# Optimization experiments

Hardware: AMD Instinct MI355X
Metric: run time of the kernel (lower is better)

## Reference

```python
import jax, jax.numpy as jnp
import numpy as np
from jax import lax

K = 9  # 3x3 kernel points


def _gather(feat, iy, ix):
    """feat: [B,C,H,W]; iy,ix: [B,K,H,W] int32. Zero padding outside bounds.
    Returns [B,C,K,H,W]."""
    B, C, H, W = feat.shape
    valid = ((iy >= 0) & (iy < H) & (ix >= 0) & (ix < W))
    iyc = jnp.clip(iy, 0, H - 1)
    ixc = jnp.clip(ix, 0, W - 1)
    flat = (iyc * W + ixc).reshape(B, 1, -1)            # [B,1,K*H*W]
    g = jnp.take_along_axis(feat.reshape(B, C, H * W), flat, axis=2)
    g = g.reshape(B, C, K, H, W)
    return g * valid[:, None].astype(feat.dtype)


def _bilinear(feat, ys, xs):
    """feat: [B,C,H,W]; ys,xs: [B,K,H,W] float sampling coords -> [B,C,K,H,W]."""
    y0 = jnp.floor(ys)
    x0 = jnp.floor(xs)
    wy = (ys - y0)[:, None]
    wx = (xs - x0)[:, None]
    y0i = y0.astype(jnp.int32)
    x0i = x0.astype(jnp.int32)
    y1i = y0i + 1
    x1i = x0i + 1
    v00 = _gather(feat, y0i, x0i)
    v01 = _gather(feat, y0i, x1i)
    v10 = _gather(feat, y1i, x0i)
    v11 = _gather(feat, y1i, x1i)
    return (v00 * (1 - wy) * (1 - wx) + v01 * (1 - wy) * wx
            + v10 * wy * (1 - wx) + v11 * wy * wx)


def _deform_layer(x, w_off, b_off, w, b, dilation=1):
    """Modulated deformable 3x3 conv, stride 1, padding=dilation (same size)."""
    B, C, H, W = x.shape
    # offset/mask conv (regular 3x3 conv, same padding)
    om = lax.conv_general_dilated(
        x, w_off, window_strides=(1, 1),
        padding=[(dilation, dilation), (dilation, dilation)],
        rhs_dilation=(dilation, dilation),
        dimension_numbers=('NCHW', 'OIHW', 'NCHW')) + b_off[None, :, None, None]
    off = om[:, :2 * K].reshape(B, K, 2, H, W)   # (dy, dx) per kernel point
    mask = jax.nn.sigmoid(om[:, 2 * K:])         # [B,K,H,W]
    dy = off[:, :, 0]
    dx = off[:, :, 1]
    # base kernel grid offsets (-d, 0, +d)
    ky, kx = jnp.meshgrid(jnp.arange(3), jnp.arange(3), indexing='ij')
    base_y = ((ky.reshape(-1) - 1) * dilation).astype(x.dtype)   # [K]
    base_x = ((kx.reshape(-1) - 1) * dilation).astype(x.dtype)
    gy = jnp.arange(H, dtype=x.dtype)
    gx = jnp.arange(W, dtype=x.dtype)
    ys = gy[None, None, :, None] + base_y[None, :, None, None] + dy  # [B,K,H,W]
    xs = gx[None, None, None, :] + base_x[None, :, None, None] + dx
    sampled = _bilinear(x, ys, xs) * mask[:, None]   # [B,C,K,H,W]
    wk = w.reshape(w.shape[0], w.shape[1], K)        # [O,I,K]
    out = jnp.einsum('bikhw,oik->bohw', sampled, wk) + b[None, :, None, None]
    return out


def setup_inputs() -> dict:
    key = jax.random.key(0)
    ks = jax.random.split(key, 16)
    B, C, H, W = 4, 256, 64, 64
    O = 256
    inp = {'x': jax.random.normal(ks[0], (B, C, H, W), jnp.float32)}
    chans = [(C, C), (C, O), (O, O)]  # layer i==num_layers-2 maps in->out
    for i, (ci, co) in enumerate(chans):
        k = jax.random.split(ks[i + 1], 4)
        # offset conv: 27 = 3*K channels (18 offsets + 9 masks); small init
        inp[f'w_off{i}'] = jax.random.normal(k[0], (3 * K, ci, 3, 3), jnp.float32) * 0.01
        inp[f'b_off{i}'] = jnp.zeros((3 * K,), jnp.float32)
        # deform conv weight: kaiming normal, fan_in = ci*K
        std = np.sqrt(2.0 / (ci * K)).astype(np.float32)
        inp[f'w{i}'] = jax.random.normal(k[1], (co, ci, 3, 3), jnp.float32) * std
        inp[f'b{i}'] = jnp.zeros((co,), jnp.float32)
    return inp


def reference(x, w_off0, b_off0, w0, b0, w_off1, b_off1, w1, b1,
              w_off2, b_off2, w2, b2):
    params = [(w_off0, b_off0, w0, b0),
              (w_off1, b_off1, w1, b1),
              (w_off2, b_off2, w2, b2)]
    for (wo, bo, w, b) in params:
        x = jax.nn.relu(_deform_layer(x, wo, bo, w, b, dilation=1))
    return x
```

## Files before the change

kernel.cpp:

```cpp
#include <hip/hip_runtime.h>
#include <math.h>

#define Bn 4
#define Cn 256
#define Hn 64
#define Wn 64
#define On 256
#define HWn 4096
#define Pn 16384
#define Kc 2304

#define LGKM0 0xc07f

typedef _Float16 half8 __attribute__((ext_vector_type(8)));
typedef float floatx4 __attribute__((ext_vector_type(4)));

__global__ void k_init(const float* __restrict__ x, _Float16* __restrict__ act0,
                       const float* __restrict__ w0, const float* __restrict__ w1,
                       const float* __restrict__ w2, const float* __restrict__ wo0,
                       const float* __restrict__ wo1, const float* __restrict__ wo2,
                       _Float16* __restrict__ wtp, _Float16* __restrict__ wbop) {
  int bx = blockIdx.x;
  int tid = threadIdx.x;
  if (bx < 4096) {
    __shared__ float tile[32][33];
    int cx = bx & 127, cy = (bx >> 7) & 7, b = bx >> 10;
    int c0 = cx * 32, r0 = cy * 32;
    int tx = tid & 31, ty = tid >> 5;
    const float* ib = x + (size_t)b * Cn * HWn;
    _Float16* ob = act0 + (size_t)b * Cn * HWn;
#pragma unroll
    for (int i = 0; i < 32; i += 8)
      tile[ty + i][tx] = ib[(size_t)(r0 + ty + i) * HWn + (c0 + tx)];
    __syncthreads();
#pragma unroll
    for (int i = 0; i < 32; i += 8)
      ob[(size_t)(c0 + ty + i) * Cn + (r0 + tx)] = (_Float16)tile[tx][ty + i];
  } else if (bx < 4864) {
    int b2 = bx - 4096;
    int l = b2 >> 8;
    int n = b2 & 255;
    const float* w = (l == 0) ? w0 : (l == 1) ? w1 : w2;
    _Float16* dst = wtp + (size_t)l * 256 * Kc;
    int g = n >> 4, col = n & 15;
    int cq = tid >> 6;
    int kk = tid & 63;
    int kq = kk >> 5;
    int k32 = kk & 31;
    int quad = k32 >> 3;
    int e = k32 & 7;
    const float* src = w + (size_t)n * 2304 + (size_t)tid * 9;
#pragma unroll
    for (int t = 0; t < 9; ++t) {
      int c = t * 4 + cq;
      size_t d = ((size_t)((c * 16 + g) * 2 + kq)) * 512 + (quad * 16 + col) * 8 + e;
      dst[d] = (_Float16)src[t];
    }
  } else {
    int b3 = bx - 4864;
    int l = b3 >> 5;
    int n = b3 & 31;
    const float* w = (l == 0) ? wo0 : (l == 1) ? wo1 : wo2;
    _Float16* dst = wbop + (size_t)l * 36 * 2048;
    int g = n >> 4, col = n & 15;
    int cw = tid >> 6;
    int r = tid & 63;
    int kq = r >> 5;
    int r2 = r & 31;
    int quad = r2 >> 3;
    int e = r2 & 7;
#pragma unroll
    for (int t = 0; t < 9; ++t) {
      int c = t * 4 + cw;
      size_t d = ((size_t)((c * 2 + g) * 2 + kq)) * 512 + (quad * 16 + col) * 8 + e;
      dst[d] = (n < 27) ? (_Float16)w[((size_t)n * 256 + tid) * 9 + t] : (_Float16)0.f;
    }
  }
}

__global__ __launch_bounds__(512) void k_layer(
    const _Float16* __restrict__ xh,
    const _Float16* __restrict__ wbop, const float* __restrict__ boff,
    const _Float16* __restrict__ wtp, const float* __restrict__ bias,
    _Float16* __restrict__ outh, float* __restrict__ outf) {
  __shared__ __align__(16) _Float16 As[2][64][72];
  __shared__ __align__(16) _Float16 Bs[2][16384];
  __shared__ __align__(16) float omS[64 * 33];
  __shared__ __align__(16) float sampS[64][9][8];

  int bid = blockIdx.x;
  int lb = ((bid & 7) << 5) + (bid >> 3);
  int p0 = lb * 64;
  int tid = threadIdx.x;
  int lane = tid & 63;
  int wave = tid >> 6;
  int quad = lane >> 4;
  int col = lane & 15;

  int ar = tid >> 3;
  int aci = (tid & 7) * 8;

  int p = p0 + ar;
  int bimg = p >> 12;
  int yx = p & 4095;
  int y = yx >> 6, x = yx & 63;

  half8 zero8;
#pragma unroll
  for (int e = 0; e < 8; ++e) zero8[e] = (_Float16)0.f;

  int mi = wave >> 1;
  int ng = wave & 1;

  floatx4 acc1 = (floatx4){0.f, 0.f, 0.f, 0.f};
  half8 ga;
  half8 bos0, bos1;
  int abase = 0;
  bool avalid = false;
  {
    int sy = y - 1, sx = x - 1;
    avalid = (sy >= 0) & (sy < Hn) & (sx >= 0) & (sx < Wn);
    abase = (((bimg * Hn + (avalid ? sy : 0)) * Wn) + (avalid ? sx : 0)) * Cn;
    ga = zero8;
    if (avalid) ga = *(const half8*)(xh + (size_t)abase + aci);
    bos0 = zero8; bos1 = zero8;
    if (tid < 256) {
      bos0 = *(const half8*)(wbop + (size_t)tid * 8);
      bos1 = *(const half8*)(wbop + 2048 + (size_t)tid * 8);
    }
  }

#pragma unroll 1
  for (int t = 0; t < 9; ++t) {
#pragma unroll
    for (int cc = 0; cc < 4; ++cc) {
      *(half8*)&As[cc & 1][ar][aci] = ga;
      if (tid < 256)
        *(half8*)&Bs[cc & 1][tid * 8] = (cc & 1) ? bos1 : bos0;
      if (cc < 3) {
        ga = zero8;
        if (avalid) ga = *(const half8*)(xh + (size_t)abase + (cc + 1) * 64 + aci);
      } else if (t < 8) {
        int tn = t + 1;
        int sy = y + tn / 3 - 1;
        int sx = x + tn % 3 - 1;
        avalid = (sy >= 0) & (sy < Hn) & (sx >= 0) & (sx < Wn);
        abase = (((bimg * Hn + (avalid ? sy : 0)) * Wn) + (avalid ? sx : 0)) * Cn;
        ga = zero8;
        if (avalid) ga = *(const half8*)(xh + (size_t)abase + aci);
      }
      if ((cc < 2 || t < 8) && tid < 256) {
        half8 v = *(const half8*)(wbop + ((size_t)(4 * t) + cc + 2) * 2048 + tid * 8);
        if (cc & 1) bos1 = v; else bos0 = v;
      }

      __builtin_amdgcn_s_waitcnt(LGKM0);
      __builtin_amdgcn_s_barrier();

#pragma unroll
      for (int kq = 0; kq < 2; ++kq) {
        half8 af = *(const half8*)&As[cc & 1][mi * 16 + col][kq * 32 + quad * 8];
        half8 bf = *(const half8*)&Bs[cc & 1][(ng * 2 + kq) * 512 + lane * 8];
        acc1 = __builtin_amdgcn_mfma_f32_16x16x32_f16(af, bf, acc1, 0, 0, 0);
      }
    }
  }

  {
    int n1 = ng * 16 + col;
    if (n1 < 27) {
      float bb = boff[n1];
#pragma unroll
      for (int r = 0; r < 4; ++r)
        omS[(mi * 16 + quad * 4 + r) * 33 + n1] = acc1[r] + bb;
    }
  }
  __syncthreads();

  for (int e = tid; e < 576; e += 512) {
    int lp = e / 9;
    int k = e - lp * 9;
    int pp = p0 + lp;
    int bi = pp >> 12;
    int pyx = pp & 4095;
    int py = pyx >> 6, px = pyx & 63;

    float dy = omS[lp * 33 + 2 * k];
    float dx = omS[lp * 33 + 2 * k + 1];
    float m = 1.f / (1.f + expf(-omS[lp * 33 + 18 + k]));

    float ys = (float)(py + k / 3 - 1) + dy;
    float xs = (float)(px + k % 3 - 1) + dx;
    float y0f = floorf(ys), x0f = floorf(xs);
    float wy = ys - y0f, wx = xs - x0f;
    int y0 = (int)y0f, x0 = (int)x0f;
    int y1 = y0 + 1, x1 = x0 + 1;

    bool vy0 = (y0 >= 0) & (y0 < Hn);
    bool vy1 = (y1 >= 0) & (y1 < Hn);
    bool vx0 = (x0 >= 0) & (x0 < Wn);
    bool vx1 = (x1 >= 0) & (x1 < Wn);
    int y0c = min(max(y0, 0), Hn - 1), y1c = min(max(y1, 0), Hn - 1);
    int x0c = min(max(x0, 0), Wn - 1), x1c = min(max(x1, 0), Wn - 1);

    int base = bi * HWn;
    float* s = &sampS[lp][k][0];
    ((int*)s)[0] = (base + y0c * Wn + x0c) * Cn;
    ((int*)s)[1] = (base + y0c * Wn + x1c) * Cn;
    ((int*)s)[2] = (base + y1c * Wn + x0c) * Cn;
    ((int*)s)[3] = (base + y1c * Wn + x1c) * Cn;
    s[4] = (vy0 && vx0) ? m * (1.f - wy) * (1.f - wx) : 0.f;
    s[5] = (vy0 && vx1) ? m * (1.f - wy) * wx : 0.f;
    s[6] = (vy1 && vx0) ? m * wy * (1.f - wx) : 0.f;
    s[7] = (vy1 && vx1) ? m * wy * wx : 0.f;
  }
  __syncthreads();

  int mw = wave >> 2;
  int nw = wave & 3;

  float bj[4];
#pragma unroll
  for (int j = 0; j < 4; ++j) bj[j] = bias[(nw * 4 + j) * 16 + col];

  floatx4 acc[2][4];
#pragma unroll
  for (int i = 0; i < 2; ++i)
#pragma unroll
    for (int j = 0; j < 4; ++j) acc[i][j] = (floatx4){0.f, 0.f, 0.f, 0.f};

  half8 g00, g01, g10, g11;
  half8 bst0[4], bst1[4];
  int4 ofsC, ofsN;
  float4 wvC, wvN;

  ofsC = *(const int4*)&sampS[ar][0][0];
  wvC = *(const float4*)&sampS[ar][0][4];
  ofsN = ofsC; wvN = wvC;
  g00 = *(const half8*)(xh + (size_t)ofsC.x + aci);
  g01 = *(const half8*)(xh + (size_t)ofsC.y + aci);
  g10 = *(const half8*)(xh + (size_t)ofsC.z + aci);
  g11 = *(const half8*)(xh + (size_t)ofsC.w + aci);
#pragma unroll
  for (int q = 0; q < 4; ++q)
    bst0[q] = *(const half8*)(wtp + (size_t)(q * 512 + tid) * 8);
#pragma unroll
  for (int q = 0; q < 4; ++q)
    bst1[q] = *(const half8*)(wtp + 16384 + (size_t)(q * 512 + tid) * 8);

#pragma unroll 1
  for (int t = 0; t < 9; ++t) {
    if (t < 8) {
      ofsN = *(const int4*)&sampS[ar][t + 1][0];
      wvN = *(const float4*)&sampS[ar][t + 1][4];
    }
#pragma unroll
    for (int cc = 0; cc < 4; ++cc) {
      {
        _Float16 h00 = (_Float16)wvC.x, h01 = (_Float16)wvC.y;
        _Float16 h10 = (_Float16)wvC.z, h11 = (_Float16)wvC.w;
        half8 r;
#pragma unroll
        for (int e = 0; e < 8; ++e)
          r[e] = g00[e] * h00 + g01[e] * h01 + g10[e] * h10 + g11[e] * h11;
        *(half8*)&As[cc & 1][ar][aci] = r;
      }
#pragma unroll
      for (int q = 0; q < 4; ++q)
        *(half8*)&Bs[cc & 1][(q * 512 + tid) * 8] = (cc & 1) ? bst1[q] : bst0[q];
      if (cc < 3) {
        int ci = (cc + 1) * 64 + aci;
        g00 = *(const half8*)(xh + (size_t)ofsC.x + ci);
        g01 = *(const half8*)(xh + (size_t)ofsC.y + ci);
        g10 = *(const half8*)(xh + (size_t)ofsC.z + ci);
        g11 = *(const half8*)(xh + (size_t)ofsC.w + ci);
      } else if (t < 8) {
        g00 = *(const half8*)(xh + (size_t)ofsN.x + aci);
        g01 = *(const half8*)(xh + (size_t)ofsN.y + aci);
        g10 = *(const half8*)(xh + (size_t)ofsN.z + aci);
        g11 = *(const half8*)(xh + (size_t)ofsN.w + aci);
      }
      if (cc < 2 || t < 8) {
        const _Float16* wsrc = wtp + ((size_t)(4 * t) + cc + 2) * 16384;
#pragma unroll
        for (int q = 0; q < 4; ++q) {
          half8 v = *(const half8*)(wsrc + (size_t)(q * 512 + tid) * 8);
          if (cc & 1) bst1[q] = v; else bst0[q] = v;
        }
      }

      __builtin_amdgcn_s_waitcnt(LGKM0);
      __builtin_amdgcn_s_barrier();

      half8 af[2][2];
#pragma unroll
      for (int kq = 0; kq < 2; ++kq)
#pragma unroll
        for (int i = 0; i < 2; ++i)
          af[kq][i] =
              *(const half8*)&As[cc & 1][mw * 32 + i * 16 + col][kq * 32 + quad * 8];

      half8 bf[2][4];
#pragma unroll
      for (int kq = 0; kq < 2; ++kq)
#pragma unroll
        for (int j = 0; j < 4; ++j)
          bf[kq][j] =
              *(const half8*)&Bs[cc & 1][((nw * 4 + j) * 2 + kq) * 512 + lane * 8];

#pragma unroll
      for (int kq = 0; kq < 2; ++kq)
#pragma unroll
        for (int i = 0; i < 2; ++i)
#pragma unroll
          for (int j = 0; j < 4; ++j)
            acc[i][j] = __builtin_amdgcn_mfma_f32_16x16x32_f16(
                af[kq][i], bf[kq][j], acc[i][j], 0, 0, 0);
    }
    ofsC = ofsN;
    wvC = wvN;
  }

#pragma unroll
  for (int i = 0; i < 2; ++i)
#pragma unroll
    for (int j = 0; j < 4; ++j) {
      int n = (nw * 4 + j) * 16 + col;
      if (outf) {
        int pb = p0 + mw * 32 + i * 16 + quad * 4;
        int bi = pb >> 12;
        int pyx = pb & 4095;
        float4 v;
        v.x = fmaxf(acc[i][j][0] + bj[j], 0.f);
        v.y = fmaxf(acc[i][j][1] + bj[j], 0.f);
        v.z = fmaxf(acc[i][j][2] + bj[j], 0.f);
        v.w = fmaxf(acc[i][j][3] + bj[j], 0.f);
        *(float4*)(outf + ((size_t)(bi * On + n)) * HWn + pyx) = v;
      } else {
#pragma unroll
        for (int r = 0; r < 4; ++r) {
          int pp = p0 + mw * 32 + i * 16 + quad * 4 + r;
          float v = fmaxf(acc[i][j][r] + bj[j], 0.f);
          outh[(size_t)pp * On + n] = (_Float16)v;
        }
      }
    }
}

extern "C" void kernel_launch(void* const* d_in, const int* in_sizes, int n_in,
                              void* d_out, int out_size, void* d_ws, size_t ws_size,
                              hipStream_t stream) {
  (void)in_sizes; (void)n_in; (void)out_size; (void)ws_size;
  const float* x = (const float*)d_in[0];

  _Float16* act0h = (_Float16*)d_ws;
  _Float16* act1h = act0h + (size_t)Pn * Cn;
  _Float16* wbop  = act1h + (size_t)Pn * Cn;
  _Float16* wtp   = wbop + (size_t)3 * 36 * 2048;

  k_init<<<4960, 256, 0, stream>>>(
      x, act0h,
      (const float*)d_in[3], (const float*)d_in[7], (const float*)d_in[11],
      (const float*)d_in[1], (const float*)d_in[5], (const float*)d_in[9],
      wtp, wbop);

  _Float16* cur = act0h;
  _Float16* nxt = act1h;
  for (int l = 0; l < 3; ++l) {
    const float* b_off = (const float*)d_in[2 + l * 4];
    const float* b     = (const float*)d_in[4 + l * 4];
    k_layer<<<Pn / 64, 512, 0, stream>>>(
        cur, wbop + (size_t)l * 36 * 2048, b_off,
        wtp + (size_t)l * 256 * Kc, b, nxt,
        (l == 2) ? (float*)d_out : nullptr);
    _Float16* tswap = cur; cur = nxt; nxt = tswap;
  }
}
```

Before: 232.3 us.

## Split k_layer into producer waves for gather and weight staging at 1024 threads

Doubles the block to 1024 threads and specializes them. The first 512 threads do the bilinear gather or offset-conv A loads, and the other 512 load weight tiles into shared memory. The main MFMA tile is redistributed over 16 waves, each computing 2x2 fragments instead of 2x4. The aim is to overlap global weight loads with gathers and add more waves to hide latency, at the cost of more barrier participants, fewer accumulators per wave and tighter register limits from launch_bounds(1024,4).

```diff
diff --git a/kernel.cpp b/kernel.cpp
--- a/kernel.cpp
+++ b/kernel.cpp
@@ -78,7 +78,7 @@
   }
 }
 
-__global__ __launch_bounds__(512) void k_layer(
+__global__ __launch_bounds__(1024, 4) void k_layer(
     const _Float16* __restrict__ xh,
     const _Float16* __restrict__ wbop, const float* __restrict__ boff,
     const _Float16* __restrict__ wtp, const float* __restrict__ bias,
@@ -97,8 +97,10 @@
   int quad = lane >> 4;
   int col = lane & 15;
 
-  int ar = tid >> 3;
+  bool isA = tid < 512;
+  int ar = (tid & 511) >> 3;
   int aci = (tid & 7) * 8;
+  int t2 = tid & 511;
 
   int p = p0 + ar;
   int bimg = p >> 12;
@@ -109,64 +111,71 @@
 #pragma unroll
   for (int e = 0; e < 8; ++e) zero8[e] = (_Float16)0.f;
 
-  int mi = wave >> 1;
+  int mi = (wave & 7) >> 1;
   int ng = wave & 1;
 
   floatx4 acc1 = (floatx4){0.f, 0.f, 0.f, 0.f};
-  half8 ga;
-  half8 bos0, bos1;
+  half8 ga = zero8;
+  half8 bos0 = zero8, bos1 = zero8;
   int abase = 0;
   bool avalid = false;
+  bool isBo = (tid >= 512) && (tid < 768);
   {
     int sy = y - 1, sx = x - 1;
     avalid = (sy >= 0) & (sy < Hn) & (sx >= 0) & (sx < Wn);
     abase = (((bimg * Hn + (avalid ? sy : 0)) * Wn) + (avalid ? sx : 0)) * Cn;
-    ga = zero8;
-    if (avalid) ga = *(const half8*)(xh + (size_t)abase + aci);
-    bos0 = zero8; bos1 = zero8;
-    if (tid < 256) {
-      bos0 = *(const half8*)(wbop + (size_t)tid * 8);
-      bos1 = *(const half8*)(wbop + 2048 + (size_t)tid * 8);
-    }
-  }
+    if (isA && avalid) ga = *(const half8*)(xh + (size_t)abase + aci);
+    if (isBo) {
+      bos0 = *(const half8*)(wbop + (size_t)t2 * 8);
+      bos1 = *(const half8*)(wbop + 2048 + (size_t)t2 * 8);
+    }
+  }
+
+  _Float16* Bo0 = &Bs[0][0];
+  _Float16* Bo1 = &Bs[0][2048];
 
 #pragma unroll 1
   for (int t = 0; t < 9; ++t) {
 #pragma unroll
     for (int cc = 0; cc < 4; ++cc) {
-      *(half8*)&As[cc & 1][ar][aci] = ga;
-      if (tid < 256)
-        *(half8*)&Bs[cc & 1][tid * 8] = (cc & 1) ? bos1 : bos0;
-      if (cc < 3) {
-        ga = zero8;
-        if (avalid) ga = *(const half8*)(xh + (size_t)abase + (cc + 1) * 64 + aci);
-      } else if (t < 8) {
-        int tn = t + 1;
-        int sy = y + tn / 3 - 1;
-        int sx = x + tn % 3 - 1;
-        avalid = (sy >= 0) & (sy < Hn) & (sx >= 0) & (sx < Wn);
-        abase = (((bimg * Hn + (avalid ? sy : 0)) * Wn) + (avalid ? sx : 0)) * Cn;
-        ga = zero8;
-        if (avalid) ga = *(const half8*)(xh + (size_t)abase + aci);
-      }
-      if ((cc < 2 || t < 8) && tid < 256) {
-        half8 v = *(const half8*)(wbop + ((size_t)(4 * t) + cc + 2) * 2048 + tid * 8);
+      if (isA) {
+        *(half8*)&As[cc & 1][ar][aci] = ga;
+      } else if (isBo) {
+        *(half8*)&((cc & 1) ? Bo1 : Bo0)[t2 * 8] = (cc & 1) ? bos1 : bos0;
+      }
+      if (isA) {
+        if (cc < 3) {
+          ga = zero8;
+          if (avalid) ga = *(const half8*)(xh + (size_t)abase + (cc + 1) * 64 + aci);
+        } else if (t < 8) {
+          int tn = t + 1;
+          int sy = y + tn / 3 - 1;
+          int sx = x + tn % 3 - 1;
+          avalid = (sy >= 0) & (sy < Hn) & (sx >= 0) & (sx < Wn);
+          abase = (((bimg * Hn + (avalid ? sy : 0)) * Wn) + (avalid ? sx : 0)) * Cn;
+          ga = zero8;
+          if (avalid) ga = *(const half8*)(xh + (size_t)abase + aci);
+        }
+      } else if (isBo && (cc < 2 || t < 8)) {
+        half8 v = *(const half8*)(wbop + ((size_t)(4 * t) + cc + 2) * 2048 + t2 * 8);
         if (cc & 1) bos1 = v; else bos0 = v;
       }
 
       __builtin_amdgcn_s_waitcnt(LGKM0);
       __builtin_amdgcn_s_barrier();
 
-#pragma unroll
-      for (int kq = 0; kq < 2; ++kq) {
-        half8 af = *(const half8*)&As[cc & 1][mi * 16 + col][kq * 32 + quad * 8];
-        half8 bf = *(const half8*)&Bs[cc & 1][(ng * 2 + kq) * 512 + lane * 8];
-        acc1 = __builtin_amdgcn_mfma_f32_16x16x32_f16(af, bf, acc1, 0, 0, 0);
-      }
-    }
-  }
-
-  {
+      if (isA) {
+#pragma unroll
+        for (int kq = 0; kq < 2; ++kq) {
+          half8 af = *(const half8*)&As[cc & 1][mi * 16 + col][kq * 32 + quad * 8];
+          half8 bf = *(const half8*)&((cc & 1) ? Bo1 : Bo0)[(ng * 2 + kq) * 512 + lane * 8];
+          acc1 = __builtin_amdgcn_mfma_f32_16x16x32_f16(af, bf, acc1, 0, 0, 0);
+        }
+      }
+    }
+  }
+
+  if (isA) {
     int n1 = ng * 16 + col;
     if (n1 < 27) {
       float bb = boff[n1];
@@ -177,7 +186,8 @@
   }
   __syncthreads();
 
-  for (int e = tid; e < 576; e += 512) {
+  if (tid < 576) {
+    int e = tid;
     int lp = e / 9;
     int k = e - lp * 9;
     int pp = p0 + lp;
@@ -216,47 +226,50 @@
   }
   __syncthreads();
 
-  int mw = wave >> 2;
-  int nw = wave & 3;
-
-  float bj[4];
-#pragma unroll
-  for (int j = 0; j < 4; ++j) bj[j] = bias[(nw * 4 + j) * 16 + col];
-
-  floatx4 acc[2][4];
+  int mw = wave >> 3;
+  int nw = wave & 7;
+
+  float bj[2];
+#pragma unroll
+  for (int j = 0; j < 2; ++j) bj[j] = bias[(nw * 2 + j) * 16 + col];
+
+  floatx4 acc[2][2];
 #pragma unroll
   for (int i = 0; i < 2; ++i)
 #pragma unroll
-    for (int j = 0; j < 4; ++j) acc[i][j] = (floatx4){0.f, 0.f, 0.f, 0.f};
-
-  half8 g00, g01, g10, g11;
+    for (int j = 0; j < 2; ++j) acc[i][j] = (floatx4){0.f, 0.f, 0.f, 0.f};
+
+  half8 g00 = zero8, g01 = zero8, g10 = zero8, g11 = zero8;
   half8 bst0[4], bst1[4];
-  int4 ofsC, ofsN;
-  float4 wvC, wvN;
-
-  ofsC = *(const int4*)&sampS[ar][0][0];
-  wvC = *(const float4*)&sampS[ar][0][4];
-  ofsN = ofsC; wvN = wvC;
-  g00 = *(const half8*)(xh + (size_t)ofsC.x + aci);
-  g01 = *(const half8*)(xh + (size_t)ofsC.y + aci);
-  g10 = *(const half8*)(xh + (size_t)ofsC.z + aci);
-  g11 = *(const half8*)(xh + (size_t)ofsC.w + aci);
-#pragma unroll
-  for (int q = 0; q < 4; ++q)
-    bst0[q] = *(const half8*)(wtp + (size_t)(q * 512 + tid) * 8);
-#pragma unroll
-  for (int q = 0; q < 4; ++q)
-    bst1[q] = *(const half8*)(wtp + 16384 + (size_t)(q * 512 + tid) * 8);
+  int4 ofsC = {0, 0, 0, 0}, ofsN = {0, 0, 0, 0};
+  float4 wvC = {0.f, 0.f, 0.f, 0.f}, wvN = wvC;
+
+  if (isA) {
+    ofsC = *(const int4*)&sampS[ar][0][0];
+    wvC = *(const float4*)&sampS[ar][0][4];
+    ofsN = ofsC; wvN = wvC;
+    g00 = *(const half8*)(xh + (size_t)ofsC.x + aci);
+    g01 = *(const half8*)(xh + (size_t)ofsC.y + aci);
+    g10 = *(const half8*)(xh + (size_t)ofsC.z + aci);
+    g11 = *(const half8*)(xh + (size_t)ofsC.w + aci);
+  } else {
+#pragma unroll
+    for (int q = 0; q < 4; ++q)
+      bst0[q] = *(const half8*)(wtp + (size_t)(q * 512 + t2) * 8);
+#pragma unroll
+    for (int q = 0; q < 4; ++q)
+      bst1[q] = *(const half8*)(wtp + 16384 + (size_t)(q * 512 + t2) * 8);
+  }
 
 #pragma unroll 1
   for (int t = 0; t < 9; ++t) {
-    if (t < 8) {
+    if (isA && t < 8) {
       ofsN = *(const int4*)&sampS[ar][t + 1][0];
       wvN = *(const float4*)&sampS[ar][t + 1][4];
     }
 #pragma unroll
     for (int cc = 0; cc < 4; ++cc) {
-      {
+      if (isA) {
         _Float16 h00 = (_Float16)wvC.x, h01 = (_Float16)wvC.y;
         _Float16 h10 = (_Float16)wvC.z, h11 = (_Float16)wvC.w;
         half8 r;
@@ -264,27 +277,29 @@
         for (int e = 0; e < 8; ++e)
           r[e] = g00[e] * h00 + g01[e] * h01 + g10[e] * h10 + g11[e] * h11;
         *(half8*)&As[cc & 1][ar][aci] = r;
-      }
-#pragma unroll
-      for (int q = 0; q < 4; ++q)
-        *(half8*)&Bs[cc & 1][(q * 512 + tid) * 8] = (cc & 1) ? bst1[q] : bst0[q];
-      if (cc < 3) {
-        int ci = (cc + 1) * 64 + aci;
-        g00 = *(const half8*)(xh + (size_t)ofsC.x + ci);
-        g01 = *(const half8*)(xh + (size_t)ofsC.y + ci);
-        g10 = *(const half8*)(xh + (size_t)ofsC.z + ci);
-        g11 = *(const half8*)(xh + (size_t)ofsC.w + ci);
-      } else if (t < 8) {
-        g00 = *(const half8*)(xh + (size_t)ofsN.x + aci);
-        g01 = *(const half8*)(xh + (size_t)ofsN.y + aci);
-        g10 = *(const half8*)(xh + (size_t)ofsN.z + aci);
-        g11 = *(const half8*)(xh + (size_t)ofsN.w + aci);
-      }
-      if (cc < 2 || t < 8) {
+      } else {
+#pragma unroll
+        for (int q = 0; q < 4; ++q)
+          *(half8*)&Bs[cc & 1][(q * 512 + t2) * 8] = (cc & 1) ? bst1[q] : bst0[q];
+      }
+      if (isA) {
+        if (cc < 3) {
+          int ci = (cc + 1) * 64 + aci;
+          g00 = *(const half8*)(xh + (size_t)ofsC.x + ci);
+          g01 = *(const half8*)(xh + (size_t)ofsC.y + ci);
+          g10 = *(const half8*)(xh + (size_t)ofsC.z + ci);
+          g11 = *(const half8*)(xh + (size_t)ofsC.w + ci);
+        } else if (t < 8) {
+          g00 = *(const half8*)(xh + (size_t)ofsN.x + aci);
+          g01 = *(const half8*)(xh + (size_t)ofsN.y + aci);
+          g10 = *(const half8*)(xh + (size_t)ofsN.z + aci);
+          g11 = *(const half8*)(xh + (size_t)ofsN.w + aci);
+        }
+      } else if (cc < 2 || t < 8) {
         const _Float16* wsrc = wtp + ((size_t)(4 * t) + cc + 2) * 16384;
 #pragma unroll
         for (int q = 0; q < 4; ++q) {
-          half8 v = *(const half8*)(wsrc + (size_t)(q * 512 + tid) * 8);
+          half8 v = *(const half8*)(wsrc + (size_t)(q * 512 + t2) * 8);
           if (cc & 1) bst1[q] = v; else bst0[q] = v;
         }
       }
@@ -300,20 +315,20 @@
           af[kq][i] =
               *(const half8*)&As[cc & 1][mw * 32 + i * 16 + col][kq * 32 + quad * 8];
 
-      half8 bf[2][4];
+      half8 bf[2][2];
 #pragma unroll
       for (int kq = 0; kq < 2; ++kq)
 #pragma unroll
-        for (int j = 0; j < 4; ++j)
+        for (int j = 0; j < 2; ++j)
           bf[kq][j] =
-              *(const half8*)&Bs[cc & 1][((nw * 4 + j) * 2 + kq) * 512 + lane * 8];
+              *(const half8*)&Bs[cc & 1][((nw * 2 + j) * 2 + kq) * 512 + lane * 8];
 
 #pragma unroll
       for (int kq = 0; kq < 2; ++kq)
 #pragma unroll
         for (int i = 0; i < 2; ++i)
 #pragma unroll
-          for (int j = 0; j < 4; ++j)
+          for (int j = 0; j < 2; ++j)
             acc[i][j] = __builtin_amdgcn_mfma_f32_16x16x32_f16(
                 af[kq][i], bf[kq][j], acc[i][j], 0, 0, 0);
     }
@@ -324,8 +339,8 @@
 #pragma unroll
   for (int i = 0; i < 2; ++i)
 #pragma unroll
-    for (int j = 0; j < 4; ++j) {
-      int n = (nw * 4 + j) * 16 + col;
+    for (int j = 0; j < 2; ++j) {
+      int n = (nw * 2 + j) * 16 + col;
       if (outf) {
         int pb = p0 + mw * 32 + i * 16 + quad * 4;
         int bi = pb >> 12;
@@ -369,7 +384,7 @@
   for (int l = 0; l < 3; ++l) {
     const float* b_off = (const float*)d_in[2 + l * 4];
     const float* b     = (const float*)d_in[4 + l * 4];
-    k_layer<<<Pn / 64, 512, 0, stream>>>(
+    k_layer<<<Pn / 64, 1024, 0, stream>>>(
         cur, wbop + (size_t)l * 36 * 2048, b_off,
         wtp + (size_t)l * 256 * Kc, b, nxt,
         (l == 2) ? (float*)d_out : nullptr);
```

Result: no change. 232.8 us (+0.2%).

## Load main-conv weight fragments directly into registers, bypassing LDS staging

Applied to the files above, without the earlier changes.

Each wave now owns 32 output channels across all 64 pixels (4x2 MFMA tiles) and loads its B-operand weight fragments straight from global memory into registers in MFMA layout. This removes the large 64KB shared-memory B buffer, the LDS store of weights, and the LDS reads of B fragments. The trade-off is that each wave reads A for all 64 rows from LDS, and weight reads become per-wave rather than shared across the block. The smaller LDS footprint may allow more blocks to reside per CU.

```diff
diff --git a/kernel.cpp b/kernel.cpp
--- a/kernel.cpp
+++ b/kernel.cpp
@@ -84,7 +84,7 @@
     const _Float16* __restrict__ wtp, const float* __restrict__ bias,
     _Float16* __restrict__ outh, float* __restrict__ outf) {
   __shared__ __align__(16) _Float16 As[2][64][72];
-  __shared__ __align__(16) _Float16 Bs[2][16384];
+  __shared__ __align__(16) _Float16 BoS[2][2048];
   __shared__ __align__(16) float omS[64 * 33];
   __shared__ __align__(16) float sampS[64][9][8];
 
@@ -136,7 +136,7 @@
     for (int cc = 0; cc < 4; ++cc) {
       *(half8*)&As[cc & 1][ar][aci] = ga;
       if (tid < 256)
-        *(half8*)&Bs[cc & 1][tid * 8] = (cc & 1) ? bos1 : bos0;
+        *(half8*)&BoS[cc & 1][tid * 8] = (cc & 1) ? bos1 : bos0;
       if (cc < 3) {
         ga = zero8;
         if (avalid) ga = *(const half8*)(xh + (size_t)abase + (cc + 1) * 64 + aci);
@@ -160,7 +160,7 @@
 #pragma unroll
       for (int kq = 0; kq < 2; ++kq) {
         half8 af = *(const half8*)&As[cc & 1][mi * 16 + col][kq * 32 + quad * 8];
-        half8 bf = *(const half8*)&Bs[cc & 1][(ng * 2 + kq) * 512 + lane * 8];
+        half8 bf = *(const half8*)&BoS[cc & 1][(ng * 2 + kq) * 512 + lane * 8];
         acc1 = __builtin_amdgcn_mfma_f32_16x16x32_f16(af, bf, acc1, 0, 0, 0);
       }
     }
@@ -216,21 +216,18 @@
   }
   __syncthreads();
 
-  int mw = wave >> 2;
-  int nw = wave & 3;
-
-  float bj[4];
-#pragma unroll
-  for (int j = 0; j < 4; ++j) bj[j] = bias[(nw * 4 + j) * 16 + col];
-
-  floatx4 acc[2][4];
-#pragma unroll
-  for (int i = 0; i < 2; ++i)
-#pragma unroll
-    for (int j = 0; j < 4; ++j) acc[i][j] = (floatx4){0.f, 0.f, 0.f, 0.f};
+  float bj[2];
+#pragma unroll
+  for (int j = 0; j < 2; ++j) bj[j] = bias[(wave * 2 + j) * 16 + col];
+
+  floatx4 acc[4][2];
+#pragma unroll
+  for (int i = 0; i < 4; ++i)
+#pragma unroll
+    for (int j = 0; j < 2; ++j) acc[i][j] = (floatx4){0.f, 0.f, 0.f, 0.f};
 
   half8 g00, g01, g10, g11;
-  half8 bst0[4], bst1[4];
+  half8 bwA[2][2], bwB[2][2];
   int4 ofsC, ofsN;
   float4 wvC, wvN;
 
@@ -242,11 +239,14 @@
   g10 = *(const half8*)(xh + (size_t)ofsC.z + aci);
   g11 = *(const half8*)(xh + (size_t)ofsC.w + aci);
 #pragma unroll
-  for (int q = 0; q < 4; ++q)
-    bst0[q] = *(const half8*)(wtp + (size_t)(q * 512 + tid) * 8);
-#pragma unroll
-  for (int q = 0; q < 4; ++q)
-    bst1[q] = *(const half8*)(wtp + 16384 + (size_t)(q * 512 + tid) * 8);
+  for (int kq = 0; kq < 2; ++kq)
+#pragma unroll
+    for (int j = 0; j < 2; ++j) {
+      bwA[kq][j] = *(const half8*)(wtp +
+          (size_t)((wave * 2 + j) * 2 + kq) * 512 + lane * 8);
+      bwB[kq][j] = *(const half8*)(wtp + 16384 +
+          (size_t)((wave * 2 + j) * 2 + kq) * 512 + lane * 8);
+    }
 
 #pragma unroll 1
   for (int t = 0; t < 9; ++t) {
@@ -265,9 +265,6 @@
           r[e] = g00[e] * h00 + g01[e] * h01 + g10[e] * h10 + g11[e] * h11;
         *(half8*)&As[cc & 1][ar][aci] = r;
       }
-#pragma unroll
-      for (int q = 0; q < 4; ++q)
-        *(half8*)&Bs[cc & 1][(q * 512 + tid) * 8] = (cc & 1) ? bst1[q] : bst0[q];
       if (cc < 3) {
         int ci = (cc + 1) * 64 + aci;
         g00 = *(const half8*)(xh + (size_t)ofsC.x + ci);
@@ -280,54 +277,50 @@
         g10 = *(const half8*)(xh + (size_t)ofsN.z + aci);
         g11 = *(const half8*)(xh + (size_t)ofsN.w + aci);
       }
+
+      __builtin_amdgcn_s_waitcnt(LGKM0);
+      __builtin_amdgcn_s_barrier();
+
+      half8 af[2][4];
+#pragma unroll
+      for (int kq = 0; kq < 2; ++kq)
+#pragma unroll
+        for (int i = 0; i < 4; ++i)
+          af[kq][i] =
+              *(const half8*)&As[cc & 1][i * 16 + col][kq * 32 + quad * 8];
+
+#pragma unroll
+      for (int kq = 0; kq < 2; ++kq)
+#pragma unroll
+        for (int i = 0; i < 4; ++i)
+#pragma unroll
+          for (int j = 0; j < 2; ++j)
+            acc[i][j] = __builtin_amdgcn_mfma_f32_16x16x32_f16(
+                af[kq][i], (cc & 1) ? bwB[kq][j] : bwA[kq][j], acc[i][j], 0, 0, 0);
+
       if (cc < 2 || t < 8) {
         const _Float16* wsrc = wtp + ((size_t)(4 * t) + cc + 2) * 16384;
 #pragma unroll
-        for (int q = 0; q < 4; ++q) {
-          half8 v = *(const half8*)(wsrc + (size_t)(q * 512 + tid) * 8);
-          if (cc & 1) bst1[q] = v; else bst0[q] = v;
-        }
-      }
-
-      __builtin_amdgcn_s_waitcnt(LGKM0);
-      __builtin_amdgcn_s_barrier();
-
-      half8 af[2][2];
-#pragma unroll
-      for (int kq = 0; kq < 2; ++kq)
-#pragma unroll
-        for (int i = 0; i < 2; ++i)
-          af[kq][i] =
-              *(const half8*)&As[cc & 1][mw * 32 + i * 16 + col][kq * 32 + quad * 8];
-
-      half8 bf[2][4];
-#pragma unroll
-      for (int kq = 0; kq < 2; ++kq)
-#pragma unroll
-        for (int j = 0; j < 4; ++j)
-          bf[kq][j] =
-              *(const half8*)&Bs[cc & 1][((nw * 4 + j) * 2 + kq) * 512 + lane * 8];
-
-#pragma unroll
-      for (int kq = 0; kq < 2; ++kq)
-#pragma unroll
-        for (int i = 0; i < 2; ++i)
-#pragma unroll
-          for (int j = 0; j < 4; ++j)
-            acc[i][j] = __builtin_amdgcn_mfma_f32_16x16x32_f16(
-                af[kq][i], bf[kq][j], acc[i][j], 0, 0, 0);
+        for (int kq = 0; kq < 2; ++kq)
+#pragma unroll
+          for (int j = 0; j < 2; ++j) {
+            half8 v = *(const half8*)(wsrc +
+                (size_t)((wave * 2 + j) * 2 + kq) * 512 + lane * 8);
+            if (cc & 1) bwB[kq][j] = v; else bwA[kq][j] = v;
+          }
+      }
     }
     ofsC = ofsN;
     wvC = wvN;
   }
 
 #pragma unroll
-  for (int i = 0; i < 2; ++i)
-#pragma unroll
-    for (int j = 0; j < 4; ++j) {
-      int n = (nw * 4 + j) * 16 + col;
+  for (int i = 0; i < 4; ++i)
+#pragma unroll
+    for (int j = 0; j < 2; ++j) {
+      int n = (wave * 2 + j) * 16 + col;
       if (outf) {
-        int pb = p0 + mw * 32 + i * 16 + quad * 4;
+        int pb = p0 + i * 16 + quad * 4;
         int bi = pb >> 12;
         int pyx = pb & 4095;
         float4 v;
@@ -339,7 +332,7 @@
       } else {
 #pragma unroll
         for (int r = 0; r < 4; ++r) {
-          int pp = p0 + mw * 32 + i * 16 + quad * 4 + r;
+          int pp = p0 + i * 16 + quad * 4 + r;
           float v = fmaxf(acc[i][j][r] + bj[j], 0.f);
           outh[(size_t)pp * On + n] = (_Float16)v;
         }
```

Result: no change. 230.6 us (-0.7%).

## Stage 3-row halo window in LDS for offset conv, stream weights via registers

Applied to the files above, without the earlier changes.

The offset/mask 3x3 conv now loads a swizzled 3x66 pixel halo window per 64-channel group into shared memory once and reuses it across all 9 taps. Before, it re-gathered the shifted input rows from global memory for every tap. Offset weights are reordered to channel-group-major layout and read straight into registers, double-buffered per tap, so the Bs staging and its per-step barriers go away. The cost is an extra 25KB of LDS, which may reduce occupancy.

```diff
diff --git a/kernel.cpp b/kernel.cpp
--- a/kernel.cpp
+++ b/kernel.cpp
@@ -71,7 +71,7 @@
     int e = r2 & 7;
 #pragma unroll
     for (int t = 0; t < 9; ++t) {
-      int c = t * 4 + cw;
+      int c = cw * 9 + t;
       size_t d = ((size_t)((c * 2 + g) * 2 + kq)) * 512 + (quad * 16 + col) * 8 + e;
       dst[d] = (n < 27) ? (_Float16)w[((size_t)n * 256 + tid) * 9 + t] : (_Float16)0.f;
     }
@@ -85,6 +85,7 @@
     _Float16* __restrict__ outh, float* __restrict__ outf) {
   __shared__ __align__(16) _Float16 As[2][64][72];
   __shared__ __align__(16) _Float16 Bs[2][16384];
+  __shared__ __align__(16) _Float16 win[3 * 66 * 64];
   __shared__ __align__(16) float omS[64 * 33];
   __shared__ __align__(16) float sampS[64][9][8];
 
@@ -100,10 +101,8 @@
   int ar = tid >> 3;
   int aci = (tid & 7) * 8;
 
-  int p = p0 + ar;
-  int bimg = p >> 12;
-  int yx = p & 4095;
-  int y = yx >> 6, x = yx & 63;
+  int yB = (p0 & 4095) >> 6;
+  int bB = p0 >> 12;
 
   half8 zero8;
 #pragma unroll
@@ -113,57 +112,54 @@
   int ng = wave & 1;
 
   floatx4 acc1 = (floatx4){0.f, 0.f, 0.f, 0.f};
-  half8 ga;
-  half8 bos0, bos1;
-  int abase = 0;
-  bool avalid = false;
-  {
-    int sy = y - 1, sx = x - 1;
-    avalid = (sy >= 0) & (sy < Hn) & (sx >= 0) & (sx < Wn);
-    abase = (((bimg * Hn + (avalid ? sy : 0)) * Wn) + (avalid ? sx : 0)) * Cn;
-    ga = zero8;
-    if (avalid) ga = *(const half8*)(xh + (size_t)abase + aci);
-    bos0 = zero8; bos1 = zero8;
-    if (tid < 256) {
-      bos0 = *(const half8*)(wbop + (size_t)tid * 8);
-      bos1 = *(const half8*)(wbop + 2048 + (size_t)tid * 8);
-    }
+  half8 boA[2], boB[2];
+#pragma unroll
+  for (int kq = 0; kq < 2; ++kq) {
+    boA[kq] = *(const half8*)(wbop + (size_t)(ng * 2 + kq) * 512 + lane * 8);
+    boB[kq] = *(const half8*)(wbop + 2048 + (size_t)(ng * 2 + kq) * 512 + lane * 8);
   }
 
 #pragma unroll 1
-  for (int t = 0; t < 9; ++t) {
-#pragma unroll
-    for (int cc = 0; cc < 4; ++cc) {
-      *(half8*)&As[cc & 1][ar][aci] = ga;
-      if (tid < 256)
-        *(half8*)&Bs[cc & 1][tid * 8] = (cc & 1) ? bos1 : bos0;
-      if (cc < 3) {
-        ga = zero8;
-        if (avalid) ga = *(const half8*)(xh + (size_t)abase + (cc + 1) * 64 + aci);
-      } else if (t < 8) {
-        int tn = t + 1;
-        int sy = y + tn / 3 - 1;
-        int sx = x + tn % 3 - 1;
-        avalid = (sy >= 0) & (sy < Hn) & (sx >= 0) & (sx < Wn);
-        abase = (((bimg * Hn + (avalid ? sy : 0)) * Wn) + (avalid ? sx : 0)) * Cn;
-        ga = zero8;
-        if (avalid) ga = *(const half8*)(xh + (size_t)abase + aci);
-      }
-      if ((cc < 2 || t < 8) && tid < 256) {
-        half8 v = *(const half8*)(wbop + ((size_t)(4 * t) + cc + 2) * 2048 + tid * 8);
-        if (cc & 1) bos1 = v; else bos0 = v;
-      }
-
-      __builtin_amdgcn_s_waitcnt(LGKM0);
-      __builtin_amdgcn_s_barrier();
-
+  for (int cg = 0; cg < 4; ++cg) {
+    for (int e = tid; e < 1584; e += 512) {
+      int seg = e & 7;
+      int rowpx = e >> 3;
+      int r = rowpx / 66;
+      int px = rowpx - r * 66;
+      int yy = yB + r - 1;
+      int xx = px - 1;
+      half8 v = zero8;
+      if (((unsigned)yy < 64u) & ((unsigned)xx < 64u))
+        v = *(const half8*)(xh + ((size_t)((bB * Hn + yy) * Wn + xx)) * Cn +
+                            cg * 64 + seg * 8);
+      int ba = (rowpx * 128 + seg * 16) ^ ((px & 7) << 4);
+      *(half8*)((char*)win + ba) = v;
+    }
+    __syncthreads();
+
+#pragma unroll
+    for (int t = 0; t < 9; ++t) {
+      int cp = cg * 9 + t;
+      int dty = t / 3;
+      int dtx = t % 3;
 #pragma unroll
       for (int kq = 0; kq < 2; ++kq) {
-        half8 af = *(const half8*)&As[cc & 1][mi * 16 + col][kq * 32 + quad * 8];
-        half8 bf = *(const half8*)&Bs[cc & 1][(ng * 2 + kq) * 512 + lane * 8];
-        acc1 = __builtin_amdgcn_mfma_f32_16x16x32_f16(af, bf, acc1, 0, 0, 0);
-      }
-    }
+        int pxw = mi * 16 + col + dtx;
+        int ba = ((dty * 66 + pxw) * 128 + kq * 64 + quad * 16) ^ ((pxw & 7) << 4);
+        half8 af = *(const half8*)((const char*)win + ba);
+        acc1 = __builtin_amdgcn_mfma_f32_16x16x32_f16(
+            af, (cp & 1) ? boB[kq] : boA[kq], acc1, 0, 0, 0);
+      }
+      if (cp + 2 < 36) {
+        const _Float16* wob = wbop + (size_t)(cp + 2) * 2048;
+#pragma unroll
+        for (int kq = 0; kq < 2; ++kq) {
+          half8 v2 = *(const half8*)(wob + (size_t)(ng * 2 + kq) * 512 + lane * 8);
+          if (cp & 1) boB[kq] = v2; else boA[kq] = v2;
+        }
+      }
+    }
+    __syncthreads();
   }
 
   {
```

Measured after the change: 230.8 us. No clear change (-0.6%).
